# Performance work log

Hardware: AMD Instinct MI355X
Metric: run time of the kernel (lower is better)

## Reference

```python
import jax, jax.numpy as jnp
import numpy as np

EMBED_DIM = 1024
NUM_HEADS = 16
HEAD_DIM = EMBED_DIM // NUM_HEADS


def setup_inputs() -> dict:
    key = jax.random.key(0)
    ks = jax.random.split(key, 7)
    B, L, E = 2, 2048, EMBED_DIM
    scale = 1.0 / np.sqrt(E)
    x = jax.random.normal(ks[0], (B, L, E), dtype=jnp.float32)
    Wq = jax.random.normal(ks[1], (E, E), dtype=jnp.float32) * scale
    Wk = jax.random.normal(ks[2], (E, E), dtype=jnp.float32) * scale
    Wv = jax.random.normal(ks[3], (E, E), dtype=jnp.float32) * scale
    bq = jax.random.normal(ks[4], (E,), dtype=jnp.float32) * 0.01
    bk = jax.random.normal(ks[5], (E,), dtype=jnp.float32) * 0.01
    bv = jax.random.normal(ks[6], (E,), dtype=jnp.float32) * 0.01
    return {"x": x, "Wq": Wq, "bq": bq, "Wk": Wk, "bk": bk, "Wv": Wv, "bv": bv}


def reference(x, Wq, bq, Wk, bk, Wv, bv):
    B, L, E = x.shape
    H, D = NUM_HEADS, HEAD_DIM

    def proj(W, b):
        # [B,L,E] -> [B,H,L,D]
        return (x @ W + b).reshape(B, L, H, D).transpose(0, 2, 1, 3)

    q = proj(Wq, bq)
    k = proj(Wk, bk)
    v = proj(Wv, bv)
    # scores: [B,H,L,M]; NOTE: no 1/sqrt(d) scaling in the original
    scores = jnp.einsum('bhld,bhmd->bhlm', q, k)
    # softmax over the QUERY axis (dim=2), matching scores.softmax(dim=2)
    weights = jax.nn.softmax(scores, axis=2)
    out = jnp.einsum('bhlm,bhmd->bhld', weights, v)
    return out.transpose(0, 2, 1, 3).reshape(B, L, E)
```

## Files before the change

kernel.cpp:

```cpp
#include <hip/hip_runtime.h>


typedef _Float16 f16x8 __attribute__((ext_vector_type(8)));
typedef _Float16 f16x4 __attribute__((ext_vector_type(4)));
typedef __fp16 fp16x2 __attribute__((ext_vector_type(2)));
typedef float f32x4 __attribute__((ext_vector_type(4)));

#define MFMA(a, b, c) __builtin_amdgcn_mfma_f32_16x16x32_f16((a), (b), (c), 0, 0, 0)
#define EXP2(x) __builtin_amdgcn_exp2f(x)
#define LOG2E 1.44269504088896340736f

#define GLOAD_LDS(gp, lp)                                                    \
    __builtin_amdgcn_global_load_lds(                                        \
        (const __attribute__((address_space(1))) void*)(const void*)(gp),    \
        (__attribute__((address_space(3))) void*)(void*)(lp), 16, 0, 0)

__global__ __launch_bounds__(256) void k_convert_x(const float* __restrict__ x,
                                                   _Float16* __restrict__ xb) {
    int i = (blockIdx.x * 256 + threadIdx.x) * 4;
    float4 f = *(const float4*)(x + i);
    f16x4 o = {(_Float16)f.x, (_Float16)f.y, (_Float16)f.z, (_Float16)f.w};
    *(f16x4*)(xb + i) = o;
}

__global__ __launch_bounds__(256) void k_convert_wt(const float* __restrict__ Wq,
                                                    const float* __restrict__ Wk,
                                                    const float* __restrict__ Wv,
                                                    _Float16* __restrict__ wbt) {
    const int jz = blockIdx.z;
    const float* W = (jz == 0) ? Wq : (jz == 1) ? Wk : Wv;
    __shared__ float tile[64][65];
    const int k0 = blockIdx.y * 64, n0 = blockIdx.x * 64;
    for (int e = threadIdx.x; e < 4096; e += 256) {
        int r = e >> 6, c = e & 63;
        tile[r][c] = W[(k0 + r) * 1024 + n0 + c];
    }
    __syncthreads();
    for (int e = threadIdx.x; e < 4096; e += 256) {
        int r = e >> 6, c = e & 63;
        wbt[((size_t)jz * 1024 + n0 + r) * 1024 + k0 + c] = (_Float16)tile[c][r];
    }
}

__global__ __launch_bounds__(256) void k_proj_gemm(const _Float16* __restrict__ xb,
                                                   const _Float16* __restrict__ wbt,
                                                   const float* __restrict__ bq,
                                                   const float* __restrict__ bk,
                                                   const float* __restrict__ bv,
                                                   _Float16* __restrict__ Qb,
                                                   _Float16* __restrict__ Kb,
                                                   _Float16* __restrict__ Vt) {
    const int n0 = blockIdx.x * 128;
    const int m0 = blockIdx.y * 128;
    __shared__ _Float16 As[128][32];
    __shared__ _Float16 Bs[128][32];
    const int tid = threadIdx.x;
    const int lane = tid & 63, wv = tid >> 6;
    const int l15 = lane & 15, quad = lane >> 4;
    const int wr = wv >> 1, wc = wv & 1;
    const int srow = lane >> 2, scol = (lane & 3) * 8;

    f32x4 acc[4][4] = {};
    for (int k0 = 0; k0 < 1024; k0 += 32) {
        __syncthreads();
        #pragma unroll
        for (int j = 0; j < 2; ++j) {
            const int grp = j * 4 + wv;
            GLOAD_LDS(&xb[(size_t)(m0 + grp * 16 + srow) * 1024 + k0 + scol],
                      &As[grp * 16][0]);
            GLOAD_LDS(&wbt[(size_t)(n0 + grp * 16 + srow) * 1024 + k0 + scol],
                      &Bs[grp * 16][0]);
        }
        __syncthreads();
        f16x8 af[4], bf[4];
        #pragma unroll
        for (int i = 0; i < 4; ++i) {
            af[i] = *(const f16x8*)&As[wr * 64 + i * 16 + l15][quad * 8];
            bf[i] = *(const f16x8*)&Bs[wc * 64 + i * 16 + l15][quad * 8];
        }
        #pragma unroll
        for (int i = 0; i < 4; ++i)
            #pragma unroll
            for (int j = 0; j < 4; ++j)
                acc[i][j] = MFMA(af[i], bf[j], acc[i][j]);
    }

    const int proj = n0 >> 10;
    const float* bias = (proj == 0) ? bq : (proj == 1) ? bk : bv;
    const float scale = (proj == 0) ? LOG2E : 1.0f;
    for (int j = 0; j < 4; ++j) {
        int n = n0 + wc * 64 + j * 16 + l15;
        int nn = n & 1023;
        float bsv = bias[nn];
        int h = nn >> 6, d = nn & 63;
        for (int i = 0; i < 4; ++i) {
            for (int r = 0; r < 4; ++r) {
                int t = m0 + wr * 64 + i * 16 + quad * 4 + r;
                int b = t >> 11, l = t & 2047;
                _Float16 val = (_Float16)((acc[i][j][r] + bsv) * scale);
                int bh = b * 16 + h;
                if (proj == 0)
                    Qb[((size_t)bh * 2048 + l) * 64 + d] = val;
                else if (proj == 1)
                    Kb[((size_t)bh * 2048 + l) * 64 + d] = val;
                else
                    Vt[((size_t)bh * 64 + d) * 2048 + l] = val;
            }
        }
    }
}

__global__ __launch_bounds__(256, 2) void k_stats(const _Float16* __restrict__ Qb,
                                                  const _Float16* __restrict__ Kb,
                                                  float* __restrict__ d2) {
    __shared__ _Float16 Qs[128][64];
    __shared__ float sred[4][4][64];
    const int id = blockIdx.x;
    const int wk = (id & 7) * 128 + (id >> 3);
    const int bh = wk >> 5;
    const int mt = wk & 31;
    const int lane = threadIdx.x & 63, wv = threadIdx.x >> 6;
    const int l15 = lane & 15, quad = lane >> 4;
    const int m0 = mt * 64;
    const size_t base = (size_t)bh * 2048 * 64;
    const _Float16* Kp = Kb + base;
    const _Float16* Qp = Qb + base;
    const int sw = l15 & 7;

    f16x8 bf[4][2];
    #pragma unroll
    for (int s = 0; s < 4; ++s) {
        bf[s][0] = *(const f16x8*)&Kp[(size_t)(m0 + s * 16 + l15) * 64 + quad * 8];
        bf[s][1] = *(const f16x8*)&Kp[(size_t)(m0 + s * 16 + l15) * 64 + 32 + quad * 8];
    }
    int qoff[4];
    #pragma unroll
    for (int j = 0; j < 4; ++j) {
        int r = (4 * wv + j) * 8 + (lane >> 3);
        int ss = (lane & 7) ^ (r & 7);
        qoff[j] = r * 64 + ss * 8;
    }
    float rs[4] = {0.f, 0.f, 0.f, 0.f};

    for (int ch = 0; ch < 16; ++ch) {
        const _Float16* qc = Qp + (size_t)ch * 8192;
        #pragma unroll
        for (int j = 0; j < 4; ++j)
            GLOAD_LDS(qc + qoff[j], &Qs[(4 * wv + j) * 8][0]);
        __syncthreads();
        __builtin_amdgcn_s_setprio(1);
        #pragma unroll
        for (int lt = 0; lt < 2; ++lt) {
            const int row = wv * 32 + lt * 16 + l15;
            f16x8 q0 = *(const f16x8*)&Qs[row][((0 + quad) ^ sw) * 8];
            f16x8 q1 = *(const f16x8*)&Qs[row][((4 + quad) ^ sw) * 8];
            #pragma unroll
            for (int s = 0; s < 4; ++s) {
                f32x4 a = {};
                a = MFMA(q0, bf[s][0], a);
                a = MFMA(q1, bf[s][1], a);
                rs[s] += EXP2(a[0]) + EXP2(a[1]) + EXP2(a[2]) + EXP2(a[3]);
            }
        }
        __builtin_amdgcn_s_setprio(0);
        __syncthreads();
    }

    #pragma unroll
    for (int s = 0; s < 4; ++s) sred[wv][s][lane] = rs[s];
    __syncthreads();
    if (wv == 0) {
        #pragma unroll
        for (int s = 0; s < 4; ++s) {
            float t = sred[0][s][lane] + sred[1][s][lane] + sred[2][s][lane] + sred[3][s][lane];
            t += __shfl_xor(t, 16, 64);
            t += __shfl_xor(t, 32, 64);
            rs[s] = t;
        }
        float myz = (quad == 0) ? rs[0] : (quad == 1) ? rs[1] : (quad == 2) ? rs[2] : rs[3];
        d2[bh * 2048 + m0 + quad * 16 + l15] = __builtin_amdgcn_logf(myz);
    }
}

__global__ __launch_bounds__(256, 2) void k_attn(const _Float16* __restrict__ Qb,
                                                 const _Float16* __restrict__ Kb,
                                                 const _Float16* __restrict__ Vt,
                                                 const float* __restrict__ d2,
                                                 float* __restrict__ out) {
    __shared__ _Float16 Ks[64][64];
    __shared__ _Float16 Vs[64][64];
    __shared__ float d2s[2048];
    const int id = blockIdx.x;
    const int wk = (id & 7) * 64 + (id >> 3);
    const int bh = wk >> 4;
    const int ltile = wk & 15;
    const int b = bh >> 4, h = bh & 15;
    const int lane = threadIdx.x & 63, wv = threadIdx.x >> 6;
    const int l15 = lane & 15, quad = lane >> 4;
    const int lw = ltile * 128 + wv * 32;
    const size_t base = (size_t)bh * 2048 * 64;
    const _Float16* Qp = Qb + base;
    const _Float16* Kp = Kb + base;
    const _Float16* Vp = Vt + base;
    const float* d2p = d2 + bh * 2048;
    const int sw = l15 & 7;
    const int srcA = (l15 + ((quad & 1) << 5)) << 2;
    const int srcB = srcA + 64;
    const bool slo = (quad < 2);

    GLOAD_LDS(d2p + (2 * wv) * 256 + lane * 4, &d2s[(2 * wv) * 256]);
    GLOAD_LDS(d2p + (2 * wv + 1) * 256 + lane * 4, &d2s[(2 * wv + 1) * 256]);

    f16x8 qf[2][2];
    #pragma unroll
    for (int lt = 0; lt < 2; ++lt) {
        qf[lt][0] = *(const f16x8*)&Qp[(size_t)(lw + lt * 16 + l15) * 64 + quad * 8];
        qf[lt][1] = *(const f16x8*)&Qp[(size_t)(lw + lt * 16 + l15) * 64 + 32 + quad * 8];
    }
    f32x4 oacc[4][2] = {};

    const int r0 = 16 * wv + (lane >> 3), r1 = r0 + 8;
    const int ss0 = (lane & 7) ^ (r0 & 7), ss1 = (lane & 7) ^ (r1 & 7);
    const size_t ko0 = (size_t)r0 * 64 + ss0 * 8, ko1 = (size_t)r1 * 64 + ss1 * 8;
    const size_t vo0 = (size_t)r0 * 2048 + ss0 * 8, vo1 = (size_t)r1 * 2048 + ss1 * 8;

    for (int ch = 0; ch < 32; ++ch) {
        const _Float16* kc = Kp + (size_t)ch * 4096;
        const _Float16* vc = Vp + ch * 64;
        GLOAD_LDS(kc + ko0, &Ks[16 * wv][0]);
        GLOAD_LDS(kc + ko1, &Ks[16 * wv + 8][0]);
        GLOAD_LDS(vc + vo0, &Vs[16 * wv][0]);
        GLOAD_LDS(vc + vo1, &Vs[16 * wv + 8][0]);
        __syncthreads();
        __builtin_amdgcn_s_setprio(1);
        #pragma unroll
        for (int sub = 0; sub < 2; ++sub) {
            f32x4 dvv[2];
            #pragma unroll
            for (int s = 0; s < 2; ++s)
                dvv[s] = *(const f32x4*)&d2s[ch * 64 + sub * 32 + s * 16 + quad * 4];
            f16x8 kf[2][2];
            #pragma unroll
            for (int s = 0; s < 2; ++s) {
                const int row = sub * 32 + s * 16 + l15;
                kf[s][0] = *(const f16x8*)&Ks[row][((0 + quad) ^ sw) * 8];
                kf[s][1] = *(const f16x8*)&Ks[row][((4 + quad) ^ sw) * 8];
            }
            f16x8 vfr[4];
            #pragma unroll
            for (int dt = 0; dt < 4; ++dt)
                vfr[dt] = *(const f16x8*)&Vs[dt * 16 + l15][((sub * 4 + quad) ^ sw) * 8];
            #pragma unroll
            for (int lt = 0; lt < 2; ++lt) {
                unsigned int c[2][2];
                #pragma unroll
                for (int s = 0; s < 2; ++s) {
                    f32x4 a = {};
                    a = MFMA(kf[s][0], qf[lt][0], a);
                    a = MFMA(kf[s][1], qf[lt][1], a);
                    union { fp16x2 hh; unsigned int u; } u0, u1;
                    u0.hh = __builtin_amdgcn_cvt_pkrtz(EXP2(a[0] - dvv[s][0]),
                                                       EXP2(a[1] - dvv[s][1]));
                    u1.hh = __builtin_amdgcn_cvt_pkrtz(EXP2(a[2] - dvv[s][2]),
                                                       EXP2(a[3] - dvv[s][3]));
                    c[s][0] = u0.u;
                    c[s][1] = u1.u;
                }
                int t0a = __builtin_amdgcn_ds_bpermute(srcA, (int)c[0][0]);
                int t1a = __builtin_amdgcn_ds_bpermute(srcA, (int)c[1][0]);
                int t0b = __builtin_amdgcn_ds_bpermute(srcA, (int)c[0][1]);
                int t1b = __builtin_amdgcn_ds_bpermute(srcA, (int)c[1][1]);
                int t0c = __builtin_amdgcn_ds_bpermute(srcB, (int)c[0][0]);
                int t1c = __builtin_amdgcn_ds_bpermute(srcB, (int)c[1][0]);
                int t0d = __builtin_amdgcn_ds_bpermute(srcB, (int)c[0][1]);
                int t1d = __builtin_amdgcn_ds_bpermute(srcB, (int)c[1][1]);
                union { int w[4]; f16x8 v; } pu;
                pu.w[0] = slo ? t0a : t1a;
                pu.w[1] = slo ? t0b : t1b;
                pu.w[2] = slo ? t0c : t1c;
                pu.w[3] = slo ? t0d : t1d;
                #pragma unroll
                for (int dt = 0; dt < 4; ++dt)
                    oacc[dt][lt] = MFMA(vfr[dt], pu.v, oacc[dt][lt]);
            }
        }
        __builtin_amdgcn_s_setprio(0);
        __syncthreads();
    }

    #pragma unroll
    for (int lt = 0; lt < 2; ++lt)
        #pragma unroll
        for (int dt = 0; dt < 4; ++dt) {
            int l = lw + lt * 16 + l15;
            float4 o4 = {oacc[dt][lt][0], oacc[dt][lt][1], oacc[dt][lt][2], oacc[dt][lt][3]};
            *(float4*)&out[((size_t)(b * 2048 + l)) * 1024 + h * 64 + dt * 16 + quad * 4] = o4;
        }
}

extern "C" void kernel_launch(void* const* d_in, const int* in_sizes, int n_in,
                              void* d_out, int out_size, void* d_ws, size_t ws_size,
                              hipStream_t stream) {
    const float* x  = (const float*)d_in[0];
    const float* Wq = (const float*)d_in[1];
    const float* bq = (const float*)d_in[2];
    const float* Wk = (const float*)d_in[3];
    const float* bk = (const float*)d_in[4];
    const float* Wv = (const float*)d_in[5];
    const float* bv = (const float*)d_in[6];
    float* out = (float*)d_out;

    char* w = (char*)d_ws;
    _Float16* xb  = (_Float16*)(w);
    _Float16* wbt = (_Float16*)(w + (size_t)(8 << 20));
    _Float16* Qb  = (_Float16*)(w + (size_t)(14 << 20));
    _Float16* Kb  = (_Float16*)(w + (size_t)(22 << 20));
    _Float16* Vt  = (_Float16*)(w + (size_t)(30 << 20));
    float* d2     = (float*)(w + (size_t)(38 << 20));

    k_convert_x<<<4096, 256, 0, stream>>>(x, xb);
    k_convert_wt<<<dim3(16, 16, 3), 256, 0, stream>>>(Wq, Wk, Wv, wbt);
    k_proj_gemm<<<dim3(24, 32), 256, 0, stream>>>(xb, wbt, bq, bk, bv, Qb, Kb, Vt);
    k_stats<<<1024, 256, 0, stream>>>(Qb, Kb, d2);
    k_attn<<<512, 256, 0, stream>>>(Qb, Kb, Vt, d2, out);
}
```

Before: 216.1 us.

## Double-buffer LDS tiles in stats and attention kernels to overlap loads with compute

Both the stats kernel (Q chunks) and the attention kernel (K/V chunks) now use two LDS buffers. The next chunk's async global-to-LDS load is issued before computing on the current buffer, so load latency can be hidden behind the MFMA/exp work. This doubles the LDS footprint per block, which may reduce occupancy. It relies on the barrier placement to keep buffers from being overwritten while in use.

```diff
diff --git a/kernel.cpp b/kernel.cpp
--- a/kernel.cpp
+++ b/kernel.cpp
@@ -113,7 +113,7 @@
 __global__ __launch_bounds__(256, 2) void k_stats(const _Float16* __restrict__ Qb,
                                                   const _Float16* __restrict__ Kb,
                                                   float* __restrict__ d2) {
-    __shared__ _Float16 Qs[128][64];
+    __shared__ _Float16 Qs[2][128][64];
     __shared__ float sred[4][4][64];
     const int id = blockIdx.x;
     const int wk = (id & 7) * 128 + (id >> 3);
@@ -142,29 +142,43 @@
     }
     float rs[4] = {0.f, 0.f, 0.f, 0.f};
 
-    for (int ch = 0; ch < 16; ++ch) {
-        const _Float16* qc = Qp + (size_t)ch * 8192;
-        #pragma unroll
-        for (int j = 0; j < 4; ++j)
-            GLOAD_LDS(qc + qoff[j], &Qs[(4 * wv + j) * 8][0]);
-        __syncthreads();
-        __builtin_amdgcn_s_setprio(1);
-        #pragma unroll
-        for (int lt = 0; lt < 2; ++lt) {
-            const int row = wv * 32 + lt * 16 + l15;
-            f16x8 q0 = *(const f16x8*)&Qs[row][((0 + quad) ^ sw) * 8];
-            f16x8 q1 = *(const f16x8*)&Qs[row][((4 + quad) ^ sw) * 8];
-            #pragma unroll
-            for (int s = 0; s < 4; ++s) {
-                f32x4 a = {};
-                a = MFMA(q0, bf[s][0], a);
-                a = MFMA(q1, bf[s][1], a);
-                rs[s] += EXP2(a[0]) + EXP2(a[1]) + EXP2(a[2]) + EXP2(a[3]);
-            }
-        }
-        __builtin_amdgcn_s_setprio(0);
-        __syncthreads();
-    }
+#define SSTAGE(P, CH) do {                                                   \
+        const _Float16* qc_ = Qp + (size_t)(CH) * 8192;                      \
+        _Pragma("unroll")                                                    \
+        for (int j = 0; j < 4; ++j)                                          \
+            GLOAD_LDS(qc_ + qoff[j], &Qs[P][(4 * wv + j) * 8][0]);           \
+    } while (0)
+
+#define SCOMP(P) do {                                                        \
+        __builtin_amdgcn_s_setprio(1);                                       \
+        _Pragma("unroll")                                                    \
+        for (int lt = 0; lt < 2; ++lt) {                                     \
+            const int row = wv * 32 + lt * 16 + l15;                         \
+            f16x8 q0 = *(const f16x8*)&Qs[P][row][((0 + quad) ^ sw) * 8];    \
+            f16x8 q1 = *(const f16x8*)&Qs[P][row][((4 + quad) ^ sw) * 8];    \
+            _Pragma("unroll")                                                \
+            for (int s = 0; s < 4; ++s) {                                    \
+                f32x4 a = {};                                                \
+                a = MFMA(q0, bf[s][0], a);                                   \
+                a = MFMA(q1, bf[s][1], a);                                   \
+                rs[s] += EXP2(a[0]) + EXP2(a[1]) + EXP2(a[2]) + EXP2(a[3]);  \
+            }                                                                \
+        }                                                                    \
+        __builtin_amdgcn_s_setprio(0);                                       \
+    } while (0)
+
+    SSTAGE(0, 0);
+    __syncthreads();
+    for (int ch = 0; ch < 16; ch += 2) {
+        SSTAGE(1, ch + 1);
+        SCOMP(0);
+        __syncthreads();
+        if (ch + 2 < 16) SSTAGE(0, ch + 2);
+        SCOMP(1);
+        __syncthreads();
+    }
+#undef SSTAGE
+#undef SCOMP
 
     #pragma unroll
     for (int s = 0; s < 4; ++s) sred[wv][s][lane] = rs[s];
@@ -187,8 +201,8 @@
                                                  const _Float16* __restrict__ Vt,
                                                  const float* __restrict__ d2,
                                                  float* __restrict__ out) {
-    __shared__ _Float16 Ks[64][64];
-    __shared__ _Float16 Vs[64][64];
+    __shared__ _Float16 Ks[2][64][64];
+    __shared__ _Float16 Vs[2][64][64];
     __shared__ float d2s[2048];
     const int id = blockIdx.x;
     const int wk = (id & 7) * 64 + (id >> 3);
@@ -224,69 +238,83 @@
     const size_t ko0 = (size_t)r0 * 64 + ss0 * 8, ko1 = (size_t)r1 * 64 + ss1 * 8;
     const size_t vo0 = (size_t)r0 * 2048 + ss0 * 8, vo1 = (size_t)r1 * 2048 + ss1 * 8;
 
-    for (int ch = 0; ch < 32; ++ch) {
-        const _Float16* kc = Kp + (size_t)ch * 4096;
-        const _Float16* vc = Vp + ch * 64;
-        GLOAD_LDS(kc + ko0, &Ks[16 * wv][0]);
-        GLOAD_LDS(kc + ko1, &Ks[16 * wv + 8][0]);
-        GLOAD_LDS(vc + vo0, &Vs[16 * wv][0]);
-        GLOAD_LDS(vc + vo1, &Vs[16 * wv + 8][0]);
-        __syncthreads();
-        __builtin_amdgcn_s_setprio(1);
-        #pragma unroll
-        for (int sub = 0; sub < 2; ++sub) {
-            f32x4 dvv[2];
-            #pragma unroll
-            for (int s = 0; s < 2; ++s)
-                dvv[s] = *(const f32x4*)&d2s[ch * 64 + sub * 32 + s * 16 + quad * 4];
-            f16x8 kf[2][2];
-            #pragma unroll
-            for (int s = 0; s < 2; ++s) {
-                const int row = sub * 32 + s * 16 + l15;
-                kf[s][0] = *(const f16x8*)&Ks[row][((0 + quad) ^ sw) * 8];
-                kf[s][1] = *(const f16x8*)&Ks[row][((4 + quad) ^ sw) * 8];
-            }
-            f16x8 vfr[4];
-            #pragma unroll
-            for (int dt = 0; dt < 4; ++dt)
-                vfr[dt] = *(const f16x8*)&Vs[dt * 16 + l15][((sub * 4 + quad) ^ sw) * 8];
-            #pragma unroll
-            for (int lt = 0; lt < 2; ++lt) {
-                unsigned int c[2][2];
-                #pragma unroll
-                for (int s = 0; s < 2; ++s) {
-                    f32x4 a = {};
-                    a = MFMA(kf[s][0], qf[lt][0], a);
-                    a = MFMA(kf[s][1], qf[lt][1], a);
-                    union { fp16x2 hh; unsigned int u; } u0, u1;
-                    u0.hh = __builtin_amdgcn_cvt_pkrtz(EXP2(a[0] - dvv[s][0]),
-                                                       EXP2(a[1] - dvv[s][1]));
-                    u1.hh = __builtin_amdgcn_cvt_pkrtz(EXP2(a[2] - dvv[s][2]),
-                                                       EXP2(a[3] - dvv[s][3]));
-                    c[s][0] = u0.u;
-                    c[s][1] = u1.u;
-                }
-                int t0a = __builtin_amdgcn_ds_bpermute(srcA, (int)c[0][0]);
-                int t1a = __builtin_amdgcn_ds_bpermute(srcA, (int)c[1][0]);
-                int t0b = __builtin_amdgcn_ds_bpermute(srcA, (int)c[0][1]);
-                int t1b = __builtin_amdgcn_ds_bpermute(srcA, (int)c[1][1]);
-                int t0c = __builtin_amdgcn_ds_bpermute(srcB, (int)c[0][0]);
-                int t1c = __builtin_amdgcn_ds_bpermute(srcB, (int)c[1][0]);
-                int t0d = __builtin_amdgcn_ds_bpermute(srcB, (int)c[0][1]);
-                int t1d = __builtin_amdgcn_ds_bpermute(srcB, (int)c[1][1]);
-                union { int w[4]; f16x8 v; } pu;
-                pu.w[0] = slo ? t0a : t1a;
-                pu.w[1] = slo ? t0b : t1b;
-                pu.w[2] = slo ? t0c : t1c;
-                pu.w[3] = slo ? t0d : t1d;
-                #pragma unroll
-                for (int dt = 0; dt < 4; ++dt)
-                    oacc[dt][lt] = MFMA(vfr[dt], pu.v, oacc[dt][lt]);
-            }
-        }
-        __builtin_amdgcn_s_setprio(0);
-        __syncthreads();
-    }
+#define ASTAGE(P, CH) do {                                                   \
+        const _Float16* kc_ = Kp + (size_t)(CH) * 4096;                      \
+        const _Float16* vc_ = Vp + (CH) * 64;                                \
+        GLOAD_LDS(kc_ + ko0, &Ks[P][16 * wv][0]);                            \
+        GLOAD_LDS(kc_ + ko1, &Ks[P][16 * wv + 8][0]);                        \
+        GLOAD_LDS(vc_ + vo0, &Vs[P][16 * wv][0]);                            \
+        GLOAD_LDS(vc_ + vo1, &Vs[P][16 * wv + 8][0]);                        \
+    } while (0)
+
+#define ACOMP(P, CH) do {                                                     \
+        __builtin_amdgcn_s_setprio(1);                                        \
+        _Pragma("unroll")                                                     \
+        for (int sub = 0; sub < 2; ++sub) {                                   \
+            f32x4 dvv[2];                                                     \
+            _Pragma("unroll")                                                 \
+            for (int s = 0; s < 2; ++s)                                       \
+                dvv[s] = *(const f32x4*)&d2s[(CH) * 64 + sub * 32 + s * 16 + quad * 4]; \
+            f16x8 kf[2][2];                                                   \
+            _Pragma("unroll")                                                 \
+            for (int s = 0; s < 2; ++s) {                                     \
+                const int row = sub * 32 + s * 16 + l15;                      \
+                kf[s][0] = *(const f16x8*)&Ks[P][row][((0 + quad) ^ sw) * 8]; \
+                kf[s][1] = *(const f16x8*)&Ks[P][row][((4 + quad) ^ sw) * 8]; \
+            }                                                                 \
+            f16x8 vfr[4];                                                     \
+            _Pragma("unroll")                                                 \
+            for (int dt = 0; dt < 4; ++dt)                                    \
+                vfr[dt] = *(const f16x8*)&Vs[P][dt * 16 + l15][((sub * 4 + quad) ^ sw) * 8]; \
+            _Pragma("unroll")                                                 \
+            for (int lt = 0; lt < 2; ++lt) {                                  \
+                unsigned int c[2][2];                                         \
+                _Pragma("unroll")                                             \
+                for (int s = 0; s < 2; ++s) {                                 \
+                    f32x4 a = {};                                             \
+                    a = MFMA(kf[s][0], qf[lt][0], a);                         \
+                    a = MFMA(kf[s][1], qf[lt][1], a);                         \
+                    union { fp16x2 hh; unsigned int u; } u0, u1;              \
+                    u0.hh = __builtin_amdgcn_cvt_pkrtz(EXP2(a[0] - dvv[s][0]),\
+                                                       EXP2(a[1] - dvv[s][1]));\
+                    u1.hh = __builtin_amdgcn_cvt_pkrtz(EXP2(a[2] - dvv[s][2]),\
+                                                       EXP2(a[3] - dvv[s][3]));\
+                    c[s][0] = u0.u;                                           \
+                    c[s][1] = u1.u;                                           \
+                }                                                             \
+                int t0a = __builtin_amdgcn_ds_bpermute(srcA, (int)c[0][0]);   \
+                int t1a = __builtin_amdgcn_ds_bpermute(srcA, (int)c[1][0]);   \
+                int t0b = __builtin_amdgcn_ds_bpermute(srcA, (int)c[0][1]);   \
+                int t1b = __builtin_amdgcn_ds_bpermute(srcA, (int)c[1][1]);   \
+                int t0c = __builtin_amdgcn_ds_bpermute(srcB, (int)c[0][0]);   \
+                int t1c = __builtin_amdgcn_ds_bpermute(srcB, (int)c[1][0]);   \
+                int t0d = __builtin_amdgcn_ds_bpermute(srcB, (int)c[0][1]);   \
+                int t1d = __builtin_amdgcn_ds_bpermute(srcB, (int)c[1][1]);   \
+                union { int w[4]; f16x8 v; } pu;                              \
+                pu.w[0] = slo ? t0a : t1a;                                    \
+                pu.w[1] = slo ? t0b : t1b;                                    \
+                pu.w[2] = slo ? t0c : t1c;                                    \
+                pu.w[3] = slo ? t0d : t1d;                                    \
+                _Pragma("unroll")                                             \
+                for (int dt = 0; dt < 4; ++dt)                                \
+                    oacc[dt][lt] = MFMA(vfr[dt], pu.v, oacc[dt][lt]);         \
+            }                                                                 \
+        }                                                                     \
+        __builtin_amdgcn_s_setprio(0);                                        \
+    } while (0)
+
+    ASTAGE(0, 0);
+    __syncthreads();
+    for (int ch = 0; ch < 32; ch += 2) {
+        ASTAGE(1, ch + 1);
+        ACOMP(0, ch);
+        __syncthreads();
+        if (ch + 2 < 32) ASTAGE(0, ch + 2);
+        ACOMP(1, ch + 1);
+        __syncthreads();
+    }
+#undef ASTAGE
+#undef ACOMP
 
     #pragma unroll
     for (int lt = 0; lt < 2; ++lt)
```

After: 210.6 us. 1.03x faster.
